# Performance work log

Measured on AMD Instinct MI355X. Metric: run time of the kernel, lower is better.

## Reference

```python
import jax, jax.numpy as jnp
import numpy as np

EMBED_DIM = 192
N_HEADS = 8
HEAD_DIM = EMBED_DIM // N_HEADS  # 24


def setup_inputs() -> dict:
    key = jax.random.key(0)
    k1, k2, k3 = jax.random.split(key, 3)
    b, n = 32, 1024
    s_in = 1.0 / np.sqrt(EMBED_DIM)
    return {
        "x": jax.random.normal(k1, (b, n, EMBED_DIM), dtype=jnp.float32),
        "W_qkv": jax.random.normal(k2, (EMBED_DIM, 3 * EMBED_DIM), dtype=jnp.float32) * s_in,
        "b_qkv": jnp.zeros((3 * EMBED_DIM,), dtype=jnp.float32),
        "W_proj": jax.random.normal(k3, (EMBED_DIM, EMBED_DIM), dtype=jnp.float32) * s_in,
        "b_proj": jnp.zeros((EMBED_DIM,), dtype=jnp.float32),
    }


def reference(x, W_qkv, b_qkv, W_proj, b_proj):
    b, n, _ = x.shape
    qkv = x @ W_qkv + b_qkv                               # [b, n, 3*E]
    qkv = qkv.reshape(b, n, 3, N_HEADS, HEAD_DIM)
    qkv = jnp.transpose(qkv, (2, 0, 3, 1, 4))             # [3, b, h, n, d]
    q, k, v = qkv[0], qkv[1], qkv[2]
    scale = 1.0 / np.sqrt(HEAD_DIM)
    scores = jnp.einsum("bhqd,bhkd->bhqk", q, k) * scale  # [b, h, n, n]
    attn = jax.nn.softmax(scores, axis=-1)
    # dropout is identity in eval mode
    out = jnp.einsum("bhqk,bhkd->bhqd", attn, v)          # [b, h, n, d]
    out = jnp.transpose(out, (0, 2, 1, 3)).reshape(b, n, EMBED_DIM)
    return out @ W_proj + b_proj
```

## Files before the change

kernel.cpp:

```cpp
#include <hip/hip_runtime.h>
#include <hip/hip_bf16.h>
#include <math.h>

#define B_ 32
#define N_ 1024
#define E_ 192
#define H_ 8
#define D_ 24
#define DP_ 32
#define M_ (B_ * N_)
#define QK_ELEMS ((size_t)B_ * H_ * N_ * DP_)
#define SC2 0.29448889f

typedef short bf16x8 __attribute__((ext_vector_type(8)));
typedef float f32x4 __attribute__((ext_vector_type(4)));
typedef unsigned int u32;
typedef unsigned short u16;

__device__ __forceinline__ u16 bf16_rne(float x) {
    u32 u = __builtin_bit_cast(u32, x);
    u += 0x7FFFu + ((u >> 16) & 1u);
    return (u16)(u >> 16);
}
__device__ __forceinline__ u32 cvt_pk(float lo, float hi) {
    u32 r;
    asm("v_cvt_pk_bf16_f32 %0, %1, %2" : "=v"(r) : "v"(lo), "v"(hi));
    return r;
}
__device__ __forceinline__ float fast_exp2(float x) {
#if __has_builtin(__builtin_amdgcn_exp2f)
    return __builtin_amdgcn_exp2f(x);
#else
    return __expf(x * 0.6931471805599453f);
#endif
}

__global__ __launch_bounds__(256) void convert_k(const float* __restrict__ x,
                                                 const float* __restrict__ wqkv,
                                                 const float* __restrict__ wproj,
                                                 u16* __restrict__ xb,
                                                 u16* __restrict__ wqkvt,
                                                 u16* __restrict__ wprojt) {
    const int b = blockIdx.x;
    const int t = threadIdx.x;
    if (b < 3072) {
        const size_t base = ((size_t)b * 256 + t) * 8;
        const float4 a = *(const float4*)(x + base);
        const float4 c = *(const float4*)(x + base + 4);
        const uint4 o = make_uint4(cvt_pk(a.x, a.y), cvt_pk(a.z, a.w),
                                   cvt_pk(c.x, c.y), cvt_pk(c.z, c.w));
        *(uint4*)(xb + base) = o;
    } else if (b < 3072 + 432) {
        const int idx = (b - 3072) * 256 + t;
        const int n = idx / 192, k = idx - n * 192;
        wqkvt[idx] = bf16_rne(wqkv[(size_t)k * 576 + n]);
    } else {
        const int idx = (b - 3504) * 256 + t;
        const int n = idx / 192, k = idx - n * 192;
        wprojt[idx] = bf16_rne(wproj[(size_t)k * 192 + n]);
    }
}

template <int MODE>
__global__ __launch_bounds__(256) void gemm2(const u16* __restrict__ Ab,
                                             const float* __restrict__ Af,
                                             const u16* __restrict__ Bt,
                                             const float* __restrict__ bias,
                                             u16* __restrict__ qb,
                                             u16* __restrict__ kb,
                                             u16* __restrict__ vb,
                                             float* __restrict__ outp) {
    __shared__ u16 As[128 * 72];
    __shared__ u16 Bs[64 * 72];

    const int tid = threadIdx.x;
    const int w = tid >> 6, lane = tid & 63, g = lane >> 4, q15 = lane & 15;
    const int wm = w >> 1, wn = w & 1;
    const int m0 = blockIdx.y * 128, n0 = blockIdx.x * 64;

    f32x4 acc[4][2];
    #pragma unroll
    for (int i = 0; i < 4; ++i)
        #pragma unroll
        for (int j = 0; j < 2; ++j) acc[i][j] = (f32x4){0.f, 0.f, 0.f, 0.f};

    for (int k0 = 0; k0 < 192; k0 += 64) {
        if (k0) __syncthreads();
        #pragma unroll
        for (int i = 0; i < 4; ++i) {
            const int c = i * 256 + tid;
            const int row = c >> 3, slot = c & 7;
            if (MODE == 0) {
                *(bf16x8*)(As + row * 72 + slot * 8) =
                    *(const bf16x8*)(Ab + (size_t)(m0 + row) * 192 + k0 + slot * 8);
            } else {
                const float* src = Af + (size_t)(m0 + row) * 192 + k0 + slot * 8;
                const float4 f0 = *(const float4*)(src);
                const float4 f1 = *(const float4*)(src + 4);
                const uint4 o = make_uint4(cvt_pk(f0.x, f0.y), cvt_pk(f0.z, f0.w),
                                           cvt_pk(f1.x, f1.y), cvt_pk(f1.z, f1.w));
                *(uint4*)(As + row * 72 + slot * 8) = o;
            }
        }
        #pragma unroll
        for (int i = 0; i < 2; ++i) {
            const int c = i * 256 + tid;
            const int rowb = c >> 3, slot = c & 7;
            *(bf16x8*)(Bs + rowb * 72 + slot * 8) =
                *(const bf16x8*)(Bt + (size_t)(n0 + rowb) * 192 + k0 + slot * 8);
        }
        __syncthreads();
        #pragma unroll
        for (int kk = 0; kk < 2; ++kk) {
            const bf16x8 b0 = *(const bf16x8*)(Bs + (wn * 32 + q15) * 72 + kk * 32 + g * 8);
            const bf16x8 b1 = *(const bf16x8*)(Bs + (wn * 32 + 16 + q15) * 72 + kk * 32 + g * 8);
            #pragma unroll
            for (int mi = 0; mi < 4; ++mi) {
                const bf16x8 a = *(const bf16x8*)(As + (wm * 64 + mi * 16 + q15) * 72 + kk * 32 + g * 8);
                acc[mi][0] = __builtin_amdgcn_mfma_f32_16x16x32_bf16(a, b0, acc[mi][0], 0, 0, 0);
                acc[mi][1] = __builtin_amdgcn_mfma_f32_16x16x32_bf16(a, b1, acc[mi][1], 0, 0, 0);
            }
        }
    }

    if (MODE == 1) {
        #pragma unroll
        for (int mi = 0; mi < 4; ++mi) {
            const int m = m0 + wm * 64 + mi * 16 + g * 4;
            #pragma unroll
            for (int ni = 0; ni < 2; ++ni) {
                const int n = n0 + wn * 32 + ni * 16 + q15;
                const float bv = bias[n];
                #pragma unroll
                for (int r = 0; r < 4; ++r)
                    outp[(size_t)(m + r) * 192 + n] = acc[mi][ni][r] + bv;
            }
        }
        return;
    }

    const int tensor = n0 / 192;
    const int rem0 = n0 - tensor * 192;
    if (tensor < 2) {
        u16* dst = (tensor == 0) ? qb : kb;
        #pragma unroll
        for (int mi = 0; mi < 4; ++mi) {
            const int m = m0 + wm * 64 + mi * 16 + g * 4;
            #pragma unroll
            for (int ni = 0; ni < 2; ++ni) {
                const int cl = wn * 32 + ni * 16 + q15;
                const int rem = rem0 + cl;
                const int h = rem / 24, d = rem - h * 24;
                const float bv = bias[n0 + cl];
                #pragma unroll
                for (int r = 0; r < 4; ++r) {
                    const int mm = m + r;
                    const int bb = mm >> 10, nn = mm & 1023;
                    float val = acc[mi][ni][r] + bv;
                    if (tensor == 0) val *= SC2;
                    const size_t base = ((size_t)(bb * H_ + h) << 15) + ((size_t)nn << 5);
                    dst[base + d] = bf16_rne(val);
                    if (d >= 16) dst[base + d + 8] = 0;
                }
            }
        }
    } else {
        __syncthreads();
        u16* Vb = As;
        #pragma unroll
        for (int mi = 0; mi < 4; ++mi) {
            const int ml = wm * 64 + mi * 16 + g * 4;
            #pragma unroll
            for (int ni = 0; ni < 2; ++ni) {
                const int cl = wn * 32 + ni * 16 + q15;
                const float bv = bias[n0 + cl];
                #pragma unroll
                for (int r = 0; r < 4; ++r)
                    Vb[cl * 136 + ml + r] = bf16_rne(acc[mi][ni][r] + bv);
            }
        }
        __syncthreads();
        const int lc = tid >> 2, seg = tid & 3;
        const int rem = rem0 + lc;
        const int h = rem / 24, d = rem - h * 24;
        const int bb = m0 >> 10, nnb = m0 & 1023;
        const u16* src = Vb + lc * 136 + seg * 32;
        u16* gdst = vb + (((size_t)(bb * H_ + h)) << 15) + ((size_t)d << 10) + nnb + seg * 32;
        #pragma unroll
        for (int q = 0; q < 4; ++q)
            *(uint4*)(gdst + q * 8) = *(const uint4*)(src + q * 8);
    }
}

__global__ __launch_bounds__(256) void attn_mfma(const u16* __restrict__ qb,
                                                 const u16* __restrict__ kb,
                                                 const u16* __restrict__ vb,
                                                 float* __restrict__ ctx) {
    __shared__ u16 Kl[64 * 40];
    __shared__ u16 Vt[32 * 72];
    __shared__ u16 Pl[4 * 16 * 72];

    const int bh = blockIdx.x;
    const int qt = blockIdx.y;
    const int tid = threadIdx.x;
    const int w = tid >> 6;
    const int lane = tid & 63;
    const int g = lane >> 4;
    const int q15 = lane & 15;

    const u16* qg = qb + (((size_t)bh * N_ + qt * 64 + w * 16) << 5);
    const u16* kg = kb + ((size_t)bh << 15);
    const u16* vg = vb + ((size_t)bh << 15);

    const bf16x8 qf = *(const bf16x8*)(qg + (q15 << 5) + g * 8);

    f32x4 acc0 = {0.f, 0.f, 0.f, 0.f};
    f32x4 acc1 = {0.f, 0.f, 0.f, 0.f};
    float m_run = -INFINITY, l_run = 0.f;
    u16* Pw = Pl + w * 16 * 72;

    const int krow = tid >> 2, kslot = tid & 3;
    const int vrow = tid >> 3, vslot = tid & 7;

    for (int j0 = 0; j0 < N_; j0 += 64) {
        __syncthreads();
        *(bf16x8*)(Kl + krow * 40 + kslot * 8) =
            *(const bf16x8*)(kg + ((j0 + krow) << 5) + kslot * 8);
        *(bf16x8*)(Vt + vrow * 72 + vslot * 8) =
            *(const bf16x8*)(vg + (vrow << 10) + j0 + vslot * 8);
        __syncthreads();

        f32x4 s0, s1, s2, s3;
        {
            const bf16x8 kf0 = *(const bf16x8*)(Kl + (0 + q15) * 40 + g * 8);
            const bf16x8 kf1 = *(const bf16x8*)(Kl + (16 + q15) * 40 + g * 8);
            const bf16x8 kf2 = *(const bf16x8*)(Kl + (32 + q15) * 40 + g * 8);
            const bf16x8 kf3 = *(const bf16x8*)(Kl + (48 + q15) * 40 + g * 8);
            const f32x4 z = {0.f, 0.f, 0.f, 0.f};
            s0 = __builtin_amdgcn_mfma_f32_16x16x32_bf16(kf0, qf, z, 0, 0, 0);
            s1 = __builtin_amdgcn_mfma_f32_16x16x32_bf16(kf1, qf, z, 0, 0, 0);
            s2 = __builtin_amdgcn_mfma_f32_16x16x32_bf16(kf2, qf, z, 0, 0, 0);
            s3 = __builtin_amdgcn_mfma_f32_16x16x32_bf16(kf3, qf, z, 0, 0, 0);
        }
        float p[16];
        #pragma unroll
        for (int r = 0; r < 4; ++r) {
            p[0 + r]  = s0[r];
            p[4 + r]  = s1[r];
            p[8 + r]  = s2[r];
            p[12 + r] = s3[r];
        }

        const float ma = fmaxf(fmaxf(p[0], p[1]), fmaxf(p[2], p[3]));
        const float mb = fmaxf(fmaxf(p[4], p[5]), fmaxf(p[6], p[7]));
        const float mc = fmaxf(fmaxf(p[8], p[9]), fmaxf(p[10], p[11]));
        const float md = fmaxf(fmaxf(p[12], p[13]), fmaxf(p[14], p[15]));
        float mloc = fmaxf(fmaxf(ma, mb), fmaxf(mc, md));
        mloc = fmaxf(mloc, __shfl_xor(mloc, 16));
        mloc = fmaxf(mloc, __shfl_xor(mloc, 32));

        if (!__all(mloc - m_run <= 8.f)) {
            const float m_new = fmaxf(m_run, mloc);
            const float corr = fast_exp2(m_run - m_new);
            m_run = m_new;
            l_run *= corr;
            #pragma unroll
            for (int r = 0; r < 4; ++r) {
                const float c = __shfl(corr, (g << 2) | r);
                acc0[r] *= c;
                acc1[r] *= c;
            }
        }

        float psum = 0.f;
        #pragma unroll
        for (int i = 0; i < 16; ++i) {
            p[i] = fast_exp2(p[i] - m_run);
            psum += p[i];
        }
        psum += __shfl_xor(psum, 16);
        psum += __shfl_xor(psum, 32);
        l_run += psum;

        #pragma unroll
        for (int t4 = 0; t4 < 4; ++t4) {
            uint2 wv;
            wv.x = cvt_pk(p[t4 * 4 + 0], p[t4 * 4 + 1]);
            wv.y = cvt_pk(p[t4 * 4 + 2], p[t4 * 4 + 3]);
            *(uint2*)(Pw + q15 * 72 + t4 * 16 + g * 4) = wv;
        }

        #pragma unroll
        for (int hf = 0; hf < 2; ++hf) {
            const bf16x8 pa = *(const bf16x8*)(Pw + q15 * 72 + hf * 32 + g * 8);
            const bf16x8 v0 = *(const bf16x8*)(Vt + q15 * 72 + hf * 32 + g * 8);
            const bf16x8 v1 = *(const bf16x8*)(Vt + (16 + q15) * 72 + hf * 32 + g * 8);
            acc0 = __builtin_amdgcn_mfma_f32_16x16x32_bf16(pa, v0, acc0, 0, 0, 0);
            acc1 = __builtin_amdgcn_mfma_f32_16x16x32_bf16(pa, v1, acc1, 0, 0, 0);
        }
    }

    const float inv = 1.f / l_run;
    const int bb = bh >> 3, hh = bh & 7;
    #pragma unroll
    for (int r = 0; r < 4; ++r) {
        const float iv = __shfl(inv, (g << 2) | r);
        const int row = qt * 64 + w * 16 + g * 4 + r;
        float* dst = ctx + ((size_t)bb * N_ + row) * E_ + hh * D_;
        dst[q15] = acc0[r] * iv;
        if (q15 < 8) dst[16 + q15] = acc1[r] * iv;
    }
}

extern "C" void kernel_launch(void* const* d_in, const int* in_sizes, int n_in,
                              void* d_out, int out_size, void* d_ws, size_t ws_size,
                              hipStream_t stream) {
    const float* x     = (const float*)d_in[0];
    const float* Wqkv  = (const float*)d_in[1];
    const float* bqkv  = (const float*)d_in[2];
    const float* Wproj = (const float*)d_in[3];
    const float* bproj = (const float*)d_in[4];
    float* out = (float*)d_out;

    u16* xb     = (u16*)d_ws;
    u16* wqkvt  = xb + (size_t)M_ * E_;
    u16* wprojt = wqkvt + 576 * 192;
    u16* qb     = wprojt + 192 * 192;
    u16* kb     = qb + QK_ELEMS;
    u16* vb     = kb + QK_ELEMS;
    float* ctx  = (float*)(vb + QK_ELEMS);

    dim3 blk(256);
    convert_k<<<3648, blk, 0, stream>>>(x, Wqkv, Wproj, xb, wqkvt, wprojt);
    gemm2<0><<<dim3(9, 256), blk, 0, stream>>>(xb, nullptr, wqkvt, bqkv, qb, kb, vb, nullptr);
    attn_mfma<<<dim3(B_ * H_, N_ / 64), blk, 0, stream>>>(qb, kb, vb, ctx);
    gemm2<1><<<dim3(3, 256), blk, 0, stream>>>(nullptr, ctx, wprojt, bproj,
                                               nullptr, nullptr, nullptr, out);
}
```

Baseline: 221.5 us.

## Use direct global-to-LDS loads with XOR swizzle and bf16 context buffer

The GEMM tile loads now use global_load_lds (direct global-to-LDS DMA) into an XOR-swizzled unpadded layout in place of register staging with padded rows. The attention kernel writes its context output as bf16, which halves the traffic into and out of the projection GEMM and lets that GEMM share the bf16 load path. convert_k also gains blocks that pre-fill the V padding rows, including a row of ones at d=31, whose purpose in the hidden attention code is unclear. The projection input is now rounded to bf16 before it is stored rather than inside the GEMM, and the added trailing barrier per k-step adds some synchronisation.

```diff
diff --git a/kernel.cpp b/kernel.cpp
--- a/kernel.cpp
+++ b/kernel.cpp
@@ -34,13 +34,19 @@
     return __expf(x * 0.6931471805599453f);
 #endif
 }
+__device__ __forceinline__ void gload16(const void* g, void* l) {
+    __builtin_amdgcn_global_load_lds(
+        (const __attribute__((address_space(1))) void*)g,
+        (__attribute__((address_space(3))) void*)l, 16, 0, 0);
+}
 
 __global__ __launch_bounds__(256) void convert_k(const float* __restrict__ x,
                                                  const float* __restrict__ wqkv,
                                                  const float* __restrict__ wproj,
                                                  u16* __restrict__ xb,
                                                  u16* __restrict__ wqkvt,
-                                                 u16* __restrict__ wprojt) {
+                                                 u16* __restrict__ wprojt,
+                                                 u16* __restrict__ vb) {
     const int b = blockIdx.x;
     const int t = threadIdx.x;
     if (b < 3072) {
@@ -54,24 +60,32 @@
         const int idx = (b - 3072) * 256 + t;
         const int n = idx / 192, k = idx - n * 192;
         wqkvt[idx] = bf16_rne(wqkv[(size_t)k * 576 + n]);
-    } else {
+    } else if (b < 3072 + 432 + 144) {
         const int idx = (b - 3504) * 256 + t;
         const int n = idx / 192, k = idx - n * 192;
         wprojt[idx] = bf16_rne(wproj[(size_t)k * 192 + n]);
+    } else {
+        const int p = b - 3648;
+        const int bh = p >> 2;
+        const int d = 24 + ((p & 3) << 1) + ((t * 8) >> 10);
+        const int n = (t * 8) & 1023;
+        const u32 v = (d == 31) ? 0x3F803F80u : 0u;
+        const uint4 o = make_uint4(v, v, v, v);
+        *(uint4*)(vb + ((size_t)bh << 15) + ((size_t)d << 10) + n) = o;
     }
 }
 
 template <int MODE>
 __global__ __launch_bounds__(256) void gemm2(const u16* __restrict__ Ab,
-                                             const float* __restrict__ Af,
                                              const u16* __restrict__ Bt,
                                              const float* __restrict__ bias,
                                              u16* __restrict__ qb,
                                              u16* __restrict__ kb,
                                              u16* __restrict__ vb,
                                              float* __restrict__ outp) {
-    __shared__ u16 As[128 * 72];
-    __shared__ u16 Bs[64 * 72];
+    __shared__ u16 smem[128 * 64 + 64 * 64];
+    u16* As = smem;
+    u16* Bs = smem + 128 * 64;
 
     const int tid = threadIdx.x;
     const int w = tid >> 6, lane = tid & 63, g = lane >> 4, q15 = lane & 15;
@@ -85,42 +99,36 @@
         for (int j = 0; j < 2; ++j) acc[i][j] = (f32x4){0.f, 0.f, 0.f, 0.f};
 
     for (int k0 = 0; k0 < 192; k0 += 64) {
-        if (k0) __syncthreads();
-        #pragma unroll
-        for (int i = 0; i < 4; ++i) {
-            const int c = i * 256 + tid;
-            const int row = c >> 3, slot = c & 7;
-            if (MODE == 0) {
-                *(bf16x8*)(As + row * 72 + slot * 8) =
-                    *(const bf16x8*)(Ab + (size_t)(m0 + row) * 192 + k0 + slot * 8);
-            } else {
-                const float* src = Af + (size_t)(m0 + row) * 192 + k0 + slot * 8;
-                const float4 f0 = *(const float4*)(src);
-                const float4 f1 = *(const float4*)(src + 4);
-                const uint4 o = make_uint4(cvt_pk(f0.x, f0.y), cvt_pk(f0.z, f0.w),
-                                           cvt_pk(f1.x, f1.y), cvt_pk(f1.z, f1.w));
-                *(uint4*)(As + row * 72 + slot * 8) = o;
-            }
-        }
-        #pragma unroll
-        for (int i = 0; i < 2; ++i) {
-            const int c = i * 256 + tid;
-            const int rowb = c >> 3, slot = c & 7;
-            *(bf16x8*)(Bs + rowb * 72 + slot * 8) =
-                *(const bf16x8*)(Bt + (size_t)(n0 + rowb) * 192 + k0 + slot * 8);
+        #pragma unroll
+        for (int is = 0; is < 4; ++is) {
+            const int lb = w * 256 + is * 64;
+            const int li = lb + lane;
+            const int row = li >> 3;
+            const int sl = (li & 7) ^ (row & 7);
+            gload16(Ab + (size_t)(m0 + row) * 192 + k0 + sl * 8, As + lb * 8);
+        }
+        #pragma unroll
+        for (int is = 0; is < 2; ++is) {
+            const int lb = w * 128 + is * 64;
+            const int li = lb + lane;
+            const int row = li >> 3;
+            const int sl = (li & 7) ^ (row & 7);
+            gload16(Bt + (size_t)(n0 + row) * 192 + k0 + sl * 8, Bs + lb * 8);
         }
         __syncthreads();
         #pragma unroll
         for (int kk = 0; kk < 2; ++kk) {
-            const bf16x8 b0 = *(const bf16x8*)(Bs + (wn * 32 + q15) * 72 + kk * 32 + g * 8);
-            const bf16x8 b1 = *(const bf16x8*)(Bs + (wn * 32 + 16 + q15) * 72 + kk * 32 + g * 8);
+            const int sw = (kk * 4 + g) ^ (q15 & 7);
+            const bf16x8 b0 = *(const bf16x8*)(Bs + (wn * 32 + q15) * 64 + sw * 8);
+            const bf16x8 b1 = *(const bf16x8*)(Bs + (wn * 32 + 16 + q15) * 64 + sw * 8);
             #pragma unroll
             for (int mi = 0; mi < 4; ++mi) {
-                const bf16x8 a = *(const bf16x8*)(As + (wm * 64 + mi * 16 + q15) * 72 + kk * 32 + g * 8);
+                const bf16x8 a = *(const bf16x8*)(As + (wm * 64 + mi * 16 + q15) * 64 + sw * 8);
                 acc[mi][0] = __builtin_amdgcn_mfma_f32_16x16x32_bf16(a, b0, acc[mi][0], 0, 0, 0);
                 acc[mi][1] = __builtin_amdgcn_mfma_f32_16x16x32_bf16(a, b1, acc[mi][1], 0, 0, 0);
             }
         }
+        __syncthreads();
     }
 
     if (MODE == 1) {
@@ -165,8 +173,7 @@
             }
         }
     } else {
-        __syncthreads();
-        u16* Vb = As;
+        u16* Vb = smem;
         #pragma unroll
         for (int mi = 0; mi < 4; ++mi) {
             const int ml = wm * 64 + mi * 16 + g * 4;
@@ -195,7 +202,7 @@
 __global__ __launch_bounds__(256) void attn_mfma(const u16* __restrict__ qb,
                                                  const u16* __restrict__ kb,
                                                  const u16* __restrict__ vb,
-                                                 float* __restrict__ ctx) {
+                                                 u16* __restrict__ ctxb) {
     __shared__ u16 Kl[64 * 40];
     __shared__ u16 Vt[32 * 72];
     __shared__ u16 Pl[4 * 16 * 72];
@@ -306,9 +313,9 @@
     for (int r = 0; r < 4; ++r) {
         const float iv = __shfl(inv, (g << 2) | r);
         const int row = qt * 64 + w * 16 + g * 4 + r;
-        float* dst = ctx + ((size_t)bb * N_ + row) * E_ + hh * D_;
-        dst[q15] = acc0[r] * iv;
-        if (q15 < 8) dst[16 + q15] = acc1[r] * iv;
+        u16* dst = ctxb + ((size_t)bb * N_ + row) * E_ + hh * D_;
+        dst[q15] = bf16_rne(acc0[r] * iv);
+        if (q15 < 8) dst[16 + q15] = bf16_rne(acc1[r] * iv);
     }
 }
 
@@ -328,12 +335,12 @@
     u16* qb     = wprojt + 192 * 192;
     u16* kb     = qb + QK_ELEMS;
     u16* vb     = kb + QK_ELEMS;
-    float* ctx  = (float*)(vb + QK_ELEMS);
+    u16* ctxb   = vb + QK_ELEMS;
 
     dim3 blk(256);
-    convert_k<<<3648, blk, 0, stream>>>(x, Wqkv, Wproj, xb, wqkvt, wprojt);
-    gemm2<0><<<dim3(9, 256), blk, 0, stream>>>(xb, nullptr, wqkvt, bqkv, qb, kb, vb, nullptr);
-    attn_mfma<<<dim3(B_ * H_, N_ / 64), blk, 0, stream>>>(qb, kb, vb, ctx);
-    gemm2<1><<<dim3(3, 256), blk, 0, stream>>>(nullptr, ctx, wprojt, bproj,
+    convert_k<<<4672, blk, 0, stream>>>(x, Wqkv, Wproj, xb, wqkvt, wprojt, vb);
+    gemm2<0><<<dim3(9, 256), blk, 0, stream>>>(xb, wqkvt, bqkv, qb, kb, vb, nullptr);
+    attn_mfma<<<dim3(B_ * H_, N_ / 64), blk, 0, stream>>>(qb, kb, vb, ctxb);
+    gemm2<1><<<dim3(3, 256), blk, 0, stream>>>(ctxb, wprojt, bproj,
                                                nullptr, nullptr, nullptr, out);
 }
```

New measurement: 206.0 us. 7.0% less time.
